# Kernel optimization log

Hardware: AMD Instinct MI355X
Metric: run time of the kernel (lower is better)

The kernel has to match this reference:

```python
import jax, jax.numpy as jnp
import numpy as np

# lct_fk config (matches init_kwargs)
BIN_LEN = 0.01
WALL_SIZE = 2.0
C_LIGHT = 3.0e8


def _safe_sqrt(v):
    # sqrt(relu(v)) with a well-defined (zero) subgradient at v<=0
    pos = v > 0
    return jnp.where(pos, jnp.sqrt(jnp.where(pos, v, 1.0)), 0.0)


def _trilinear_zero(vol, pz, py, px):
    # vol: (D,H,W) complex64; pz/py/px: (D2,H2,W2) float pixel coords
    # Trilinear sampling with zeros padding (== F.grid_sample align_corners=False)
    D, H, W = vol.shape
    z0f = jnp.floor(pz); y0f = jnp.floor(py); x0f = jnp.floor(px)
    dz = pz - z0f; dy = py - y0f; dx = px - x0f
    z0 = z0f.astype(jnp.int32); y0 = y0f.astype(jnp.int32); x0 = x0f.astype(jnp.int32)
    out = jnp.zeros(pz.shape, vol.dtype)
    for iz, wz in ((z0, 1.0 - dz), (z0 + 1, dz)):
        for iy, wy in ((y0, 1.0 - dy), (y0 + 1, dy)):
            for ix, wx in ((x0, 1.0 - dx), (x0 + 1, dx)):
                valid = (iz >= 0) & (iz < D) & (iy >= 0) & (iy < H) & (ix >= 0) & (ix < W)
                v = vol[jnp.clip(iz, 0, D - 1), jnp.clip(iy, 0, H - 1), jnp.clip(ix, 0, W - 1)]
                w = jnp.where(valid, wz * wy * wx, 0.0)
                out = out + w * v
    return out


def setup_inputs() -> dict:
    key = jax.random.key(0)
    feture = jax.random.uniform(key, (1, 2, 128, 128, 128), dtype=jnp.float32)
    return {"feture_bxdxtxhxw": feture}


def reference(feture_bxdxtxhxw):
    b, d, T, H, W = feture_bxdxtxhxw.shape
    M, N = T, H  # temprol_grid (== crop), sptial_grid; tbes=0, tens=crop -> no temporal pad
    width = WALL_SIZE / 2.0
    trange = M * BIN_LEN  # crop * c * (bin_len/c)

    # z-weighting: (z/(M-1))^2, then sqrt(relu(.))
    gridz = (jnp.arange(M, dtype=jnp.float32) / (M - 1)).reshape(1, M, 1, 1)
    data = feture_bxdxtxhxw.reshape(b * d, T, H, W) * (gridz ** 2)
    data = _safe_sqrt(jax.nn.relu(data))

    # zero-pad to (2T,2H,2W), FFT, fftshift (roll by half == fftshift for even sizes)
    datapad = jnp.pad(data, ((0, 0), (0, M), (0, N), (0, N)))
    fre = jnp.fft.fftshift(jnp.fft.fftn(datapad, axes=(-3, -2, -1)), axes=(-3, -2, -1))

    # Stolt (f-k) warped coordinates, normalized to [-1,1]
    zdim = (jnp.arange(2 * M, dtype=jnp.float32) - M) / M
    xdim = (jnp.arange(2 * N, dtype=jnp.float32) - N) / N
    gz = zdim[:, None, None]            # varies along axis 0
    gy = xdim[None, :, None]            # varies along axis 1
    gx = xdim[None, None, :]            # varies along axis 2
    fk = (N * trange / (M * width * 4.0)) ** 2
    gznew = jnp.sqrt(fk * (gx ** 2 + gy ** 2) + gz ** 2)  # (2M,2N,2N)
    gznew = jnp.broadcast_to(gznew, (2 * M, 2 * N, 2 * N))

    # unnormalize (align_corners=False): pix = ((c+1)*size - 1)/2
    px = ((jnp.broadcast_to(gx, gznew.shape) + 1.0) * (2 * N) - 1.0) * 0.5
    py = ((jnp.broadcast_to(gy, gznew.shape) + 1.0) * (2 * N) - 1.0) * 0.5
    pz = ((gznew + 1.0) * (2 * M) - 1.0) * 0.5

    samp = jax.vmap(lambda v: _trilinear_zero(v, pz, py, px))(fre)

    # zero negative/zero frequencies along z, then Stolt Jacobian scaling
    z0pos = M + 1  # first index where zdim > 0
    zmask = (jnp.arange(2 * M) >= z0pos)[None, :, None, None]
    samp = samp * zmask
    samp = samp * (jnp.abs(gz) / (gznew + 1e-8))[None]

    samp = jnp.fft.fftshift(samp, axes=(-3, -2, -1))  # ifftshift == fftshift (even dims)
    vol = jnp.fft.ifftn(samp, axes=(-3, -2, -1))
    out = vol[:, :M, :N, :N].real
    return out.reshape(b, d, M, N, N)
```

## Files before the change

kernel.cpp:

```cpp
#include <hip/hip_runtime.h>

static constexpr size_t VS   = 8388608;
static constexpr int    ZSTR = 65536;
static constexpr int    YSTR = 256;
static constexpr size_t VSB  = 4194304;
static constexpr int    BZS  = 32768;
static constexpr int    BYS  = 128;
static constexpr int    LSTR = 261;

typedef float vf2 __attribute__((ext_vector_type(2)));
typedef _Float16 h2 __attribute__((ext_vector_type(2)));

__device__ __forceinline__ unsigned pkh(vf2 a){
    h2 h; h.x = (_Float16)a.x; h.y = (_Float16)a.y;
    return __builtin_bit_cast(unsigned, h);
}
__device__ __forceinline__ vf2 uph(unsigned u){
    h2 h = __builtin_bit_cast(h2, u);
    vf2 r; r.x = (float)h.x; r.y = (float)h.y; return r;
}

__device__ __forceinline__ vf2 cmul(vf2 a, vf2 b){
    vf2 asw; asw.x = -a.y; asw.y = a.x;
    return a*b.x + asw*b.y;
}

constexpr int BREV(int k){ return ((k&1)<<3)|((k&2)<<1)|((k&4)>>1)|((k&8)>>3); }

__device__ __forceinline__ void bf(vf2& a, vf2& b, float c, float s){
    vf2 sum = a + b;
    vf2 dif = a - b;
    vf2 dsw; dsw.x = -dif.y; dsw.y = dif.x;
    b = dif*c + dsw*s;
    a = sum;
}

template<int DIR>
__device__ __forceinline__ void fft16(vf2 r[16]){
    constexpr float D = (float)DIR;
    constexpr float C16[8] = {1.f, 0.92387953f, 0.70710678f, 0.38268343f, 0.f, -0.38268343f, -0.70710678f, -0.92387953f};
    constexpr float S16[8] = {0.f, 0.38268343f, 0.70710678f, 0.92387953f, 1.f, 0.92387953f, 0.70710678f, 0.38268343f};
#pragma unroll
    for (int j = 0; j < 8; ++j) bf(r[j], r[j+8], C16[j], D*S16[j]);
    constexpr float C8[4] = {1.f, 0.70710678f, 0.f, -0.70710678f};
    constexpr float S8[4] = {0.f, 0.70710678f, 1.f, 0.70710678f};
#pragma unroll
    for (int g = 0; g < 16; g += 8)
#pragma unroll
        for (int j = 0; j < 4; ++j) bf(r[g+j], r[g+j+4], C8[j], D*S8[j]);
#pragma unroll
    for (int g = 0; g < 16; g += 4){
        bf(r[g],   r[g+2], 1.f, 0.f);
        bf(r[g+1], r[g+3], 0.f, D);
    }
#pragma unroll
    for (int g = 0; g < 16; g += 2) bf(r[g], r[g+1], 1.f, 0.f);
}

__device__ __forceinline__ void init_tw(vf2* tw, float dir){
    int tid = threadIdx.x;
    float ang = dir * 0.0245436926f * (float)((tid >> 4)*(tid & 15));
    float s, c; __sincosf(ang, &s, &c);
    vf2 w; w.x = c; w.y = s;
    tw[tid] = w;
}

template<int DIR>
__device__ __forceinline__ void mid256t(vf2 r[16], vf2* sh8, const vf2* tw, int t, int l){
    fft16<DIR>(r);
#pragma unroll
    for (int k1 = 1; k1 < 16; ++k1)
        r[BREV(k1)] = cmul(r[BREV(k1)], tw[k1*16 + t]);
    int lr = l & 7;
    bool lo = (l < 8);
    if (lo){
#pragma unroll
        for (int k1 = 0; k1 < 16; ++k1) sh8[lr*LSTR + k1*16 + (t ^ k1)] = r[BREV(k1)];
    }
    __syncthreads();
    if (lo){
#pragma unroll
        for (int n2 = 0; n2 < 16; ++n2) r[n2] = sh8[lr*LSTR + t*16 + (n2 ^ t)];
    }
    __syncthreads();
    if (!lo){
#pragma unroll
        for (int k1 = 0; k1 < 16; ++k1) sh8[lr*LSTR + k1*16 + (t ^ k1)] = r[BREV(k1)];
    }
    __syncthreads();
    if (!lo){
#pragma unroll
        for (int n2 = 0; n2 < 16; ++n2) r[n2] = sh8[lr*LSTR + t*16 + (n2 ^ t)];
    }
    fft16<DIR>(r);
}

template<int DIR>
__device__ __forceinline__ void twiddle_reg(vf2 r[16], int t){
    float sn, cn; __sincosf((float)DIR * 0.0245436926f * (float)t, &sn, &cn);
    vf2 w; w.x = cn; w.y = sn;
    vf2 wk = w;
#pragma unroll
    for (int k1 = 1; k1 < 16; ++k1){
        r[BREV(k1)] = cmul(r[BREV(k1)], wk);
        wk = cmul(wk, w);
    }
}

__device__ __forceinline__ void wave_transpose(vf2 r[16], vf2* shw, int t, int l){
    vf2* base = shw + ((l >> 2)*2 + (l & 1))*LSTR;
    if ((l & 2) == 0){
#pragma unroll
        for (int k1 = 0; k1 < 16; ++k1) base[k1*16 + (t ^ k1)] = r[BREV(k1)];
#pragma unroll
        for (int n2 = 0; n2 < 16; ++n2) r[n2] = base[t*16 + (n2 ^ t)];
    }
    __builtin_amdgcn_sched_barrier(0);
    if ((l & 2) != 0){
#pragma unroll
        for (int k1 = 15; k1 >= 0; --k1) base[k1*16 + (t ^ k1)] = r[BREV(k1)];
#pragma unroll
        for (int n2 = 15; n2 >= 0; --n2) r[n2] = base[t*16 + (n2 ^ t)];
    }
}

template<int DIR>
__device__ __forceinline__ void mid256wr(vf2 r[16], vf2* shw, int t, int l){
    fft16<DIR>(r);
    twiddle_reg<DIR>(r, t);
    wave_transpose(r, shw, t, l);
    fft16<DIR>(r);
}

template<int DIR, int NIN, int NOUT>
__device__ __forceinline__ void fft_strided(unsigned* g, int S, float sc){
    __shared__ vf2 sh8[8*LSTR];
    __shared__ vf2 tw[256];
    int t = threadIdx.x >> 4, l = threadIdx.x & 15;
    vf2 r[16];
    vf2 zero; zero.x = 0.f; zero.y = 0.f;
#pragma unroll
    for (int n1 = 0; n1 < 16; ++n1)
        r[n1] = (n1 < NIN/16) ? uph(g[(size_t)(16*n1 + t)*S + l]) : zero;
    init_tw(tw, (float)DIR);
    __syncthreads();
    mid256t<DIR>(r, sh8, tw, t, l);
#pragma unroll
    for (int k2 = 0; k2 < 16; ++k2)
        if (k2 < NOUT/16) g[(size_t)(t + 16*k2)*S + l] = pkh(r[BREV(k2)]*sc);
}

__global__ void __launch_bounds__(256) k_p1(const float* __restrict__ in, unsigned* __restrict__ A){
    __shared__ vf2 sh8[8*LSTR];
    int tid = threadIdx.x, bid = blockIdx.x;
    int yc = bid & 7, z = (bid >> 3) & 127, v = bid >> 10;
    int t = tid & 15, l = tid >> 4;
    float gz = z * (1.0f/127.0f);
    float g2 = gz*gz;
    const float* src = in + (((size_t)(v*128 + z))*128 + yc*16 + l)*128;
    float val[8];
#pragma unroll
    for (int n1 = 0; n1 < 8; ++n1) val[n1] = src[16*n1 + t];
#pragma unroll
    for (int n1 = 0; n1 < 8; ++n1){
        float x = val[n1] * g2;
        val[n1] = x > 0.f ? sqrtf(x) : 0.f;
    }
    float part = ((val[0]+val[1]) + (val[2]+val[3])) + ((val[4]+val[5]) + (val[6]+val[7]));
    part = (t & 1) ? -part : part;
    part += __shfl_xor(part, 1);
    part += __shfl_xor(part, 2);
    part += __shfl_xor(part, 4);
    part += __shfl_xor(part, 8);
    vf2 r[16];
    vf2 zero; zero.x = 0.f; zero.y = 0.f;
#pragma unroll
    for (int n1 = 8; n1 < 16; ++n1) r[n1] = zero;
#pragma unroll
    for (int n1 = 0; n1 < 8; ++n1){
        float sn, cn; __sincosf(0.0245436926f * (float)(16*n1 + t), &sn, &cn);
        r[n1].x = val[n1] * 0.5f * (1.f + cn);
        r[n1].y = val[n1] * 0.5f * sn;
    }
    mid256wr<-1>(r, sh8, t, l);
    if (t == 0){ r[1].x = part*0.5f; r[1].y = 0.f; }
    unsigned* dst = A + (size_t)v*VS + (size_t)z*ZSTR + (size_t)(yc*16 + l)*YSTR;
#pragma unroll
    for (int k2 = 0; k2 < 16; ++k2)
        dst[t + 16*k2] = pkh(r[BREV(k2)]);
}

__global__ void __launch_bounds__(256) k_p2z(unsigned* __restrict__ A){
    int bid = blockIdx.x;
    int xb = bid & 15, y = (bid >> 4) & 127, v = bid >> 11;
    fft_strided<-1,128,128>(A + (size_t)v*VS + (size_t)y*YSTR + xb*16, ZSTR, 1.f);
}

__global__ void __launch_bounds__(256) k_p3y(unsigned* __restrict__ A){
    __shared__ vf2 sh8[8*LSTR];
    __shared__ vf2 tw[256];
    __shared__ vf2 shW[64];
    const float SC3 = 0.015625f;
    int bid = blockIdx.x;
    int xb = bid & 15, z = (bid >> 4) & 127, v = bid >> 11;
    unsigned* g = A + (size_t)v*VS + (size_t)z*ZSTR + xb*16;
    int t = threadIdx.x >> 4, l = threadIdx.x & 15;
    vf2 r[16];
    vf2 zero; zero.x = 0.f; zero.y = 0.f;
#pragma unroll
    for (int n1 = 0; n1 < 16; ++n1)
        r[n1] = (n1 < 8) ? uph(g[(size_t)(16*n1 + t)*YSTR + l]) : zero;

    vf2 part = ((r[0]+r[1]) + (r[2]+r[3])) + ((r[4]+r[5]) + (r[6]+r[7]));
    part = part * ((t & 1) ? -1.f : 1.f);
    part.x += __shfl_xor(part.x, 16);
    part.y += __shfl_xor(part.y, 16);
    part.x += __shfl_xor(part.x, 32);
    part.y += __shfl_xor(part.y, 32);
    if ((t & 3) == 0) shW[(t >> 2)*16 + l] = part;

#pragma unroll
    for (int n1 = 0; n1 < 8; ++n1){
        float sn, cn; __sincosf(0.0245436926f * (float)(16*n1 + t), &sn, &cn);
        vf2 c; c.x = 0.5f*(1.f + cn); c.y = 0.5f*sn;
        r[n1] = cmul(r[n1], c);
    }

    init_tw(tw, -1.f);
    __syncthreads();
    mid256t<-1>(r, sh8, tw, t, l);

    if (t == 0){
        vf2 S = (shW[l] + shW[16 + l]) + (shW[32 + l] + shW[48 + l]);
        r[BREV(8)] = S * 0.5f;
    }
#pragma unroll
    for (int k2 = 0; k2 < 16; ++k2)
        g[(size_t)(t + 16*k2)*YSTR + l] = pkh(r[BREV(k2)]*SC3);
}

__global__ void __launch_bounds__(256) k_p45(const unsigned* __restrict__ A, unsigned* __restrict__ B){
    __shared__ vf2 sh8[8*LSTR];
    int tid = threadIdx.x, bid = blockIdx.x;
    int yc = bid & 15, zn = (bid >> 4) & 127, v = bid >> 11;
    const unsigned* Av = A + (size_t)v*VS;
    int t = tid & 15, l = tid >> 4;
    int yn = yc*16 + l;
    float gy = (yn < 128 ? yn : yn - 256) * (1.0f/128.0f);
    float gz = zn * (1.0f/128.0f);
    float c2 = 0.1024f*gy*gy + gz*gz;
    unsigned rowoff = (unsigned)yn*YSTR;
    vf2 r[16];
#pragma unroll
    for (int n1 = 0; n1 < 16; ++n1){
        int xn = 16*n1 + t;
        float gx = (xn < 128 ? xn : xn - 256) * (1.0f/128.0f);
        float s2 = c2 + 0.1024f*gx*gx;
        float rs = __builtin_amdgcn_rsqf(s2 + 1e-12f);
        float gznew = s2 * rs;
        float pz = gznew*128.0f + 127.5f;
        int zi = (int)pz;
        float dz = pz - (float)zi;
        int zp0 = zi - 128;
        float wf = gz * rs;
        float w0 = (((unsigned)zp0     < 128u) ? (1.0f - dz) : 0.f) * wf;
        float w1 = (((unsigned)(zp0+1) < 128u) ? dz : 0.f) * wf;
        vf2 v0 = uph(Av[(size_t)((unsigned)(zp0 & 127) * ZSTR) + rowoff + xn]);
        vf2 v1 = uph(Av[(size_t)((unsigned)((zp0 + 1) & 127) * ZSTR) + rowoff + xn]);
        r[n1] = v0*w0 + v1*w1;
    }
    mid256wr<1>(r, sh8, t, l);
    unsigned* dst = B + (size_t)v*VSB + (size_t)zn*BZS + (size_t)yn*BYS;
#pragma unroll
    for (int k2 = 0; k2 < 8; ++k2)
        dst[t + 16*k2] = pkh(r[BREV(k2)]);
}

__global__ void __launch_bounds__(256) k_p6(unsigned* __restrict__ B){
    int bid = blockIdx.x;
    int xb = bid & 7, zn = (bid >> 3) & 127, v = bid >> 10;
    fft_strided<1,256,128>(B + (size_t)v*VSB + (size_t)zn*BZS + xb*16, BYS, 0.00390625f);
}

__global__ void __launch_bounds__(256) k_p7(const unsigned* __restrict__ B, float* __restrict__ out){
    __shared__ vf2 sh8[8*LSTR];
    __shared__ vf2 tw[256];
    int bid = blockIdx.x;
    int xb = bid & 7, y = (bid >> 3) & 127, v = bid >> 10;
    const unsigned* g = B + (size_t)v*VSB + (size_t)y*BYS + xb*16;
    int t = threadIdx.x >> 4, l = threadIdx.x & 15;
    vf2 r[16];
    vf2 zero; zero.x = 0.f; zero.y = 0.f;
#pragma unroll
    for (int n1 = 0; n1 < 16; ++n1)
        r[n1] = (n1 < 8) ? uph(g[(size_t)(16*n1 + t)*BZS + l]) : zero;
    init_tw(tw, 1.f);
    __syncthreads();
    mid256t<1>(r, sh8, tw, t, l);
    const float sc = 9.765625e-4f;
    float* dst = out + ((size_t)(v*128)*128 + y)*128 + xb*16 + l;
#pragma unroll
    for (int k2 = 0; k2 < 8; ++k2)
        dst[(size_t)(t + 16*k2)*16384] = r[BREV(k2)].x * sc;
}

extern "C" void kernel_launch(void* const* d_in, const int* in_sizes, int n_in,
                              void* d_out, int out_size, void* d_ws, size_t ws_size,
                              hipStream_t stream){
    const float* in = (const float*)d_in[0];
    float* out = (float*)d_out;
    unsigned* A = (unsigned*)d_ws;
    unsigned* B = A + 2*VS;
    k_p1 <<< 2048, 256, 0, stream>>>(in, A);
    k_p2z<<< 4096, 256, 0, stream>>>(A);
    k_p3y<<< 4096, 256, 0, stream>>>(A);
    k_p45<<< 4096, 256, 0, stream>>>(A, B);
    k_p6 <<< 2048, 256, 0, stream>>>(B);
    k_p7 <<< 2048, 256, 0, stream>>>(B, out);
}
```

Measured before the change: 185.0 us.

## Process two columns per thread in strided FFTs with fp16 LDS transpose

The strided z and y FFT kernels (p2z, p3y, p6, p7) now process two adjacent x-columns per thread. This widens global loads and stores to 8 bytes, halves the grid size, and shares twiddle loads across both columns. The shared-memory transpose now stores packed fp16 values instead of fp32 complex, which keeps LDS usage the same while holding twice the data. Scaling is moved onto the input or the twiddle factors. The cost is more register pressure and an extra fp16 rounding at the intermediate transpose, which may reduce accuracy and occupancy.

```diff
diff --git a/kernel.cpp b/kernel.cpp
--- a/kernel.cpp
+++ b/kernel.cpp
@@ -66,33 +66,50 @@
 }
 
 template<int DIR>
-__device__ __forceinline__ void mid256t(vf2 r[16], vf2* sh8, const vf2* tw, int t, int l){
-    fft16<DIR>(r);
-#pragma unroll
-    for (int k1 = 1; k1 < 16; ++k1)
-        r[BREV(k1)] = cmul(r[BREV(k1)], tw[k1*16 + t]);
+__device__ __forceinline__ void mid256t2(vf2 r[2][16], unsigned* shp, const vf2* tw, int t, int l){
+#pragma unroll
+    for (int c = 0; c < 2; ++c) fft16<DIR>(r[c]);
+#pragma unroll
+    for (int k1 = 1; k1 < 16; ++k1){
+        vf2 w = tw[k1*16 + t];
+        r[0][BREV(k1)] = cmul(r[0][BREV(k1)], w);
+        r[1][BREV(k1)] = cmul(r[1][BREV(k1)], w);
+    }
     int lr = l & 7;
     bool lo = (l < 8);
     if (lo){
 #pragma unroll
-        for (int k1 = 0; k1 < 16; ++k1) sh8[lr*LSTR + k1*16 + (t ^ k1)] = r[BREV(k1)];
+        for (int c = 0; c < 2; ++c)
+#pragma unroll
+            for (int k1 = 0; k1 < 16; ++k1)
+                shp[(lr*2 + c)*LSTR + k1*16 + (t ^ k1)] = pkh(r[c][BREV(k1)]);
     }
     __syncthreads();
     if (lo){
 #pragma unroll
-        for (int n2 = 0; n2 < 16; ++n2) r[n2] = sh8[lr*LSTR + t*16 + (n2 ^ t)];
+        for (int c = 0; c < 2; ++c)
+#pragma unroll
+            for (int n2 = 0; n2 < 16; ++n2)
+                r[c][n2] = uph(shp[(lr*2 + c)*LSTR + t*16 + (n2 ^ t)]);
     }
     __syncthreads();
     if (!lo){
 #pragma unroll
-        for (int k1 = 0; k1 < 16; ++k1) sh8[lr*LSTR + k1*16 + (t ^ k1)] = r[BREV(k1)];
+        for (int c = 0; c < 2; ++c)
+#pragma unroll
+            for (int k1 = 0; k1 < 16; ++k1)
+                shp[(lr*2 + c)*LSTR + k1*16 + (t ^ k1)] = pkh(r[c][BREV(k1)]);
     }
     __syncthreads();
     if (!lo){
 #pragma unroll
-        for (int n2 = 0; n2 < 16; ++n2) r[n2] = sh8[lr*LSTR + t*16 + (n2 ^ t)];
-    }
-    fft16<DIR>(r);
+        for (int c = 0; c < 2; ++c)
+#pragma unroll
+            for (int n2 = 0; n2 < 16; ++n2)
+                r[c][n2] = uph(shp[(lr*2 + c)*LSTR + t*16 + (n2 ^ t)]);
+    }
+#pragma unroll
+    for (int c = 0; c < 2; ++c) fft16<DIR>(r[c]);
 }
 
 template<int DIR>
@@ -133,21 +150,29 @@
 }
 
 template<int DIR, int NIN, int NOUT>
-__device__ __forceinline__ void fft_strided(unsigned* g, int S, float sc){
-    __shared__ vf2 sh8[8*LSTR];
+__device__ __forceinline__ void fft_strided2(unsigned* g, int S, float insc){
+    __shared__ unsigned shp[16*LSTR];
     __shared__ vf2 tw[256];
     int t = threadIdx.x >> 4, l = threadIdx.x & 15;
-    vf2 r[16];
+    vf2 r[2][16];
     vf2 zero; zero.x = 0.f; zero.y = 0.f;
 #pragma unroll
-    for (int n1 = 0; n1 < 16; ++n1)
-        r[n1] = (n1 < NIN/16) ? uph(g[(size_t)(16*n1 + t)*S + l]) : zero;
+    for (int n1 = 0; n1 < 16; ++n1){
+        if (n1 < NIN/16){
+            uint2 ld = *reinterpret_cast<const uint2*>(&g[(size_t)(16*n1 + t)*S + 2*l]);
+            r[0][n1] = uph(ld.x)*insc;
+            r[1][n1] = uph(ld.y)*insc;
+        } else { r[0][n1] = zero; r[1][n1] = zero; }
+    }
     init_tw(tw, (float)DIR);
     __syncthreads();
-    mid256t<DIR>(r, sh8, tw, t, l);
+    mid256t2<DIR>(r, shp, tw, t, l);
 #pragma unroll
     for (int k2 = 0; k2 < 16; ++k2)
-        if (k2 < NOUT/16) g[(size_t)(t + 16*k2)*S + l] = pkh(r[BREV(k2)]*sc);
+        if (k2 < NOUT/16){
+            uint2 st; st.x = pkh(r[0][BREV(k2)]); st.y = pkh(r[1][BREV(k2)]);
+            *reinterpret_cast<uint2*>(&g[(size_t)(t + 16*k2)*S + 2*l]) = st;
+        }
 }
 
 __global__ void __launch_bounds__(256) k_p1(const float* __restrict__ in, unsigned* __restrict__ A){
@@ -192,51 +217,61 @@
 
 __global__ void __launch_bounds__(256) k_p2z(unsigned* __restrict__ A){
     int bid = blockIdx.x;
-    int xb = bid & 15, y = (bid >> 4) & 127, v = bid >> 11;
-    fft_strided<-1,128,128>(A + (size_t)v*VS + (size_t)y*YSTR + xb*16, ZSTR, 1.f);
+    int xb = bid & 7, y = (bid >> 3) & 127, v = bid >> 10;
+    fft_strided2<-1,128,128>(A + (size_t)v*VS + (size_t)y*YSTR + xb*32, ZSTR, 1.f);
 }
 
 __global__ void __launch_bounds__(256) k_p3y(unsigned* __restrict__ A){
-    __shared__ vf2 sh8[8*LSTR];
+    __shared__ unsigned shp[16*LSTR];
     __shared__ vf2 tw[256];
-    __shared__ vf2 shW[64];
+    __shared__ vf2 shW[128];
     const float SC3 = 0.015625f;
     int bid = blockIdx.x;
-    int xb = bid & 15, z = (bid >> 4) & 127, v = bid >> 11;
-    unsigned* g = A + (size_t)v*VS + (size_t)z*ZSTR + xb*16;
+    int xb = bid & 7, z = (bid >> 3) & 127, v = bid >> 10;
+    unsigned* g = A + (size_t)v*VS + (size_t)z*ZSTR + xb*32;
     int t = threadIdx.x >> 4, l = threadIdx.x & 15;
-    vf2 r[16];
+    vf2 r[2][16];
     vf2 zero; zero.x = 0.f; zero.y = 0.f;
 #pragma unroll
-    for (int n1 = 0; n1 < 16; ++n1)
-        r[n1] = (n1 < 8) ? uph(g[(size_t)(16*n1 + t)*YSTR + l]) : zero;
-
-    vf2 part = ((r[0]+r[1]) + (r[2]+r[3])) + ((r[4]+r[5]) + (r[6]+r[7]));
-    part = part * ((t & 1) ? -1.f : 1.f);
-    part.x += __shfl_xor(part.x, 16);
-    part.y += __shfl_xor(part.y, 16);
-    part.x += __shfl_xor(part.x, 32);
-    part.y += __shfl_xor(part.y, 32);
-    if ((t & 3) == 0) shW[(t >> 2)*16 + l] = part;
-
+    for (int n1 = 0; n1 < 16; ++n1){
+        if (n1 < 8){
+            uint2 ld = *reinterpret_cast<const uint2*>(&g[(size_t)(16*n1 + t)*YSTR + 2*l]);
+            r[0][n1] = uph(ld.x);
+            r[1][n1] = uph(ld.y);
+        } else { r[0][n1] = zero; r[1][n1] = zero; }
+    }
+#pragma unroll
+    for (int c = 0; c < 2; ++c){
+        vf2 part = ((r[c][0]+r[c][1]) + (r[c][2]+r[c][3])) + ((r[c][4]+r[c][5]) + (r[c][6]+r[c][7]));
+        part = part * ((t & 1) ? -1.f : 1.f);
+        part.x += __shfl_xor(part.x, 16);
+        part.y += __shfl_xor(part.y, 16);
+        part.x += __shfl_xor(part.x, 32);
+        part.y += __shfl_xor(part.y, 32);
+        if ((t & 3) == 0) shW[(t >> 2)*32 + 2*l + c] = part;
+    }
 #pragma unroll
     for (int n1 = 0; n1 < 8; ++n1){
         float sn, cn; __sincosf(0.0245436926f * (float)(16*n1 + t), &sn, &cn);
-        vf2 c; c.x = 0.5f*(1.f + cn); c.y = 0.5f*sn;
-        r[n1] = cmul(r[n1], c);
-    }
-
+        vf2 c; c.x = SC3*0.5f*(1.f + cn); c.y = SC3*0.5f*sn;
+        r[0][n1] = cmul(r[0][n1], c);
+        r[1][n1] = cmul(r[1][n1], c);
+    }
     init_tw(tw, -1.f);
     __syncthreads();
-    mid256t<-1>(r, sh8, tw, t, l);
-
+    mid256t2<-1>(r, shp, tw, t, l);
     if (t == 0){
-        vf2 S = (shW[l] + shW[16 + l]) + (shW[32 + l] + shW[48 + l]);
-        r[BREV(8)] = S * 0.5f;
-    }
-#pragma unroll
-    for (int k2 = 0; k2 < 16; ++k2)
-        g[(size_t)(t + 16*k2)*YSTR + l] = pkh(r[BREV(k2)]*SC3);
+#pragma unroll
+        for (int c = 0; c < 2; ++c){
+            vf2 S = (shW[2*l + c] + shW[32 + 2*l + c]) + (shW[64 + 2*l + c] + shW[96 + 2*l + c]);
+            r[c][BREV(8)] = S * (0.5f*SC3);
+        }
+    }
+#pragma unroll
+    for (int k2 = 0; k2 < 16; ++k2){
+        uint2 st; st.x = pkh(r[0][BREV(k2)]); st.y = pkh(r[1][BREV(k2)]);
+        *reinterpret_cast<uint2*>(&g[(size_t)(t + 16*k2)*YSTR + 2*l]) = st;
+    }
 }
 
 __global__ void __launch_bounds__(256) k_p45(const unsigned* __restrict__ A, unsigned* __restrict__ B){
@@ -278,30 +313,37 @@
 
 __global__ void __launch_bounds__(256) k_p6(unsigned* __restrict__ B){
     int bid = blockIdx.x;
-    int xb = bid & 7, zn = (bid >> 3) & 127, v = bid >> 10;
-    fft_strided<1,256,128>(B + (size_t)v*VSB + (size_t)zn*BZS + xb*16, BYS, 0.00390625f);
+    int xb = bid & 3, zn = (bid >> 2) & 127, v = bid >> 9;
+    fft_strided2<1,256,128>(B + (size_t)v*VSB + (size_t)zn*BZS + xb*32, BYS, 0.00390625f);
 }
 
 __global__ void __launch_bounds__(256) k_p7(const unsigned* __restrict__ B, float* __restrict__ out){
-    __shared__ vf2 sh8[8*LSTR];
+    __shared__ unsigned shp[16*LSTR];
     __shared__ vf2 tw[256];
+    const float sc = 9.765625e-4f;
     int bid = blockIdx.x;
-    int xb = bid & 7, y = (bid >> 3) & 127, v = bid >> 10;
-    const unsigned* g = B + (size_t)v*VSB + (size_t)y*BYS + xb*16;
+    int xb = bid & 3, y = (bid >> 2) & 127, v = bid >> 9;
+    const unsigned* g = B + (size_t)v*VSB + (size_t)y*BYS + xb*32;
     int t = threadIdx.x >> 4, l = threadIdx.x & 15;
-    vf2 r[16];
+    vf2 r[2][16];
     vf2 zero; zero.x = 0.f; zero.y = 0.f;
 #pragma unroll
-    for (int n1 = 0; n1 < 16; ++n1)
-        r[n1] = (n1 < 8) ? uph(g[(size_t)(16*n1 + t)*BZS + l]) : zero;
+    for (int n1 = 0; n1 < 16; ++n1){
+        if (n1 < 8){
+            uint2 ld = *reinterpret_cast<const uint2*>(&g[(size_t)(16*n1 + t)*BZS + 2*l]);
+            r[0][n1] = uph(ld.x)*sc;
+            r[1][n1] = uph(ld.y)*sc;
+        } else { r[0][n1] = zero; r[1][n1] = zero; }
+    }
     init_tw(tw, 1.f);
     __syncthreads();
-    mid256t<1>(r, sh8, tw, t, l);
-    const float sc = 9.765625e-4f;
-    float* dst = out + ((size_t)(v*128)*128 + y)*128 + xb*16 + l;
-#pragma unroll
-    for (int k2 = 0; k2 < 8; ++k2)
-        dst[(size_t)(t + 16*k2)*16384] = r[BREV(k2)].x * sc;
+    mid256t2<1>(r, shp, tw, t, l);
+    float* dst = out + ((size_t)(v*128)*128 + y)*128 + xb*32 + 2*l;
+#pragma unroll
+    for (int k2 = 0; k2 < 8; ++k2){
+        float2 st; st.x = r[0][BREV(k2)].x; st.y = r[1][BREV(k2)].x;
+        *reinterpret_cast<float2*>(&dst[(size_t)(t + 16*k2)*16384]) = st;
+    }
 }
 
 extern "C" void kernel_launch(void* const* d_in, const int* in_sizes, int n_in,
@@ -312,9 +354,9 @@
     unsigned* A = (unsigned*)d_ws;
     unsigned* B = A + 2*VS;
     k_p1 <<< 2048, 256, 0, stream>>>(in, A);
-    k_p2z<<< 4096, 256, 0, stream>>>(A);
-    k_p3y<<< 4096, 256, 0, stream>>>(A);
+    k_p2z<<< 2048, 256, 0, stream>>>(A);
+    k_p3y<<< 2048, 256, 0, stream>>>(A);
     k_p45<<< 4096, 256, 0, stream>>>(A, B);
-    k_p6 <<< 2048, 256, 0, stream>>>(B);
-    k_p7 <<< 2048, 256, 0, stream>>>(B, out);
-}
+    k_p6 <<< 1024, 256, 0, stream>>>(B);
+    k_p7 <<< 1024, 256, 0, stream>>>(B, out);
+}
```

Measured after the change: 184.1 us (median of 2 runs). Within noise of the previous version (-0.5%).
